# Optimization experiments

Hardware: AMD Instinct MI355X
Metric: run time of the kernel (lower is better)

## Reference

```python
import jax, jax.numpy as jnp
import numpy as np

DIM = 768
HEADS = 12
HEAD_DIM = DIM // HEADS
EPS_ATTN = 1e-6
LN_EPS = 1e-5


def _piece_weight():
    # BlockDistanceConv with num_patches_per_side=16, patch_group_size=16 -> 4x4 blocks
    bps = 4
    centers = np.array([[i + 0.5, j + 0.5] for i in range(bps) for j in range(bps)], dtype=np.float32)
    d = np.linalg.norm(centers[:, None, :] - centers[None, :, :], axis=-1)
    mat = np.cos(d / d.max() * np.pi / 4.0)  # 'cos' transform
    mat = mat / mat.sum(axis=0, keepdims=True)
    return jnp.asarray(mat, dtype=jnp.float32)  # [16, 16], out = W @ x over piece channels


def setup_inputs() -> dict:
    key = jax.random.key(0)
    ks = jax.random.split(key, 4)
    B, N, W, C = 128, 16, 16, DIM
    x = jax.random.normal(ks[0], (B, N, W, C), dtype=jnp.float32)
    ln_gamma = jnp.ones((C,), dtype=jnp.float32)
    ln_beta = jnp.zeros((C,), dtype=jnp.float32)
    w_qkv = jax.random.normal(ks[1], (C, 3 * C), dtype=jnp.float32) * (C ** -0.5)
    w_out = jax.random.normal(ks[2], (C, C), dtype=jnp.float32) * (C ** -0.5)
    b_out = jnp.zeros((C,), dtype=jnp.float32)
    w_piece = _piece_weight()
    return {"x": x, "ln_gamma": ln_gamma, "ln_beta": ln_beta, "w_qkv": w_qkv,
            "w_out": w_out, "b_out": b_out, "w_piece": w_piece}


def reference(x, ln_gamma, ln_beta, w_qkv, w_out, b_out, w_piece):
    B, N, W, C = x.shape
    H, D = HEADS, HEAD_DIM
    # LayerNorm over channel dim
    mu = jnp.mean(x, axis=-1, keepdims=True)
    var = jnp.mean((x - mu) ** 2, axis=-1, keepdims=True)
    xn = (x - mu) * jax.lax.rsqrt(var + LN_EPS) * ln_gamma + ln_beta
    # qkv projection (no bias)
    qkv = xn @ w_qkv  # [B,N,W,3C]
    q, k, v = jnp.split(qkv, 3, axis=-1)
    # relu kernel feature map
    q = jax.nn.relu(q) + EPS_ATTN
    k = jax.nn.relu(k) + EPS_ATTN
    # split heads: 'b n w (h d) -> b h n w d'
    def heads(t):
        return t.reshape(B, N, W, H, D).transpose(0, 3, 1, 2, 4)
    q, k, v = heads(q), heads(k), heads(v)
    # per-window kv = k^T v  (sum over window positions w)  -> [B,H,N,D,D]
    kv = jnp.einsum('bhnwd,bhnwe->bhnde', k, v)
    # BlockDistanceConv: 1x1 conv mixing over piece dim N with fixed weights
    kv = jnp.einsum('ij,bhjde->bhide', w_piece, kv)
    # out = q @ kv  -> [B,H,N,W,D]
    out = jnp.einsum('bhnwd,bhnde->bhnwe', q, kv)
    # merge heads: 'b h n w d -> b n w (h d)'
    out = out.transpose(0, 2, 3, 1, 4).reshape(B, N, W, H * D)
    # output projection (dropout is identity in eval)
    return out @ w_out + b_out
```

## Files before the change

### kernel.cpp

```cpp
#include <hip/hip_runtime.h>

#define DIM 768
#define HEADS 12
#define TOK 32768

typedef unsigned short ushort_t;
typedef __attribute__((ext_vector_type(8))) short short8v;
typedef __attribute__((ext_vector_type(4))) float f32x4;
typedef __attribute__((ext_vector_type(4))) unsigned short us4;

__device__ __forceinline__ ushort_t f2bf(float x) {
  union { float f; unsigned u; } c; c.f = x;
  unsigned r = (c.u + 0x7FFFu + ((c.u >> 16) & 1u)) >> 16;
  return (ushort_t)r;
}

__device__ __forceinline__ void gload_lds16(const void* g, void* l) {
  __builtin_amdgcn_global_load_lds((const __attribute__((address_space(1))) void*)g,
                                   (__attribute__((address_space(3))) void*)l, 16, 0, 0);
}

#define FENCE asm volatile("" ::: "memory")
#define SCHED0 __builtin_amdgcn_sched_barrier(0)
#define BARRIER do { FENCE; SCHED0; __builtin_amdgcn_s_barrier(); SCHED0; FENCE; } while (0)
#define LGK0 asm volatile("s_waitcnt lgkmcnt(0)" ::: "memory")
#define VM0  asm volatile("s_waitcnt vmcnt(0)" ::: "memory")
#define VM3  asm volatile("s_waitcnt vmcnt(3)" ::: "memory")

__global__ __launch_bounds__(256) void ln_kernel(const float* __restrict__ x,
                                                 const float* __restrict__ g,
                                                 const float* __restrict__ be,
                                                 ushort_t* __restrict__ xn) {
  int lane = threadIdx.x & 63;
  int row = blockIdx.x * 4 + (threadIdx.x >> 6);
  const float4* rx = (const float4*)(x + (size_t)row * DIM);
  float4 v[3];
  float s = 0.f, sq = 0.f;
  #pragma unroll
  for (int c = 0; c < 3; ++c) {
    v[c] = rx[lane + 64 * c];
    s  += v[c].x + v[c].y + v[c].z + v[c].w;
    sq += v[c].x * v[c].x + v[c].y * v[c].y + v[c].z * v[c].z + v[c].w * v[c].w;
  }
  #pragma unroll
  for (int off = 32; off; off >>= 1) {
    s  += __shfl_xor(s, off);
    sq += __shfl_xor(sq, off);
  }
  float mu  = s * (1.0f / DIM);
  float var = sq * (1.0f / DIM) - mu * mu;
  float rs  = rsqrtf(var + 1e-5f);
  us4* orow = (us4*)(xn + (size_t)row * DIM);
  const float4* gv = (const float4*)g;
  const float4* bv = (const float4*)be;
  #pragma unroll
  for (int c = 0; c < 3; ++c) {
    float4 gg = gv[lane + 64 * c];
    float4 bb = bv[lane + 64 * c];
    us4 pk;
    pk[0] = f2bf((v[c].x - mu) * rs * gg.x + bb.x);
    pk[1] = f2bf((v[c].y - mu) * rs * gg.y + bb.y);
    pk[2] = f2bf((v[c].z - mu) * rs * gg.z + bb.z);
    pk[3] = f2bf((v[c].w - mu) * rs * gg.w + bb.w);
    orow[lane + 64 * c] = pk;
  }
}

__global__ __launch_bounds__(256) void convT2(const float* __restrict__ s0,
                                              ushort_t* __restrict__ d0,
                                              const float* __restrict__ s1,
                                              ushort_t* __restrict__ d1) {
  int z = blockIdx.z;
  if (z && blockIdx.x >= DIM / 32) return;
  const float* src = z ? s1 : s0;
  ushort_t* dst = z ? d1 : d0;
  int Ccol = z ? DIM : 3 * DIM;
  const int R = DIM;
  __shared__ float tile[32][33];
  int c0 = blockIdx.x * 32, r0 = blockIdx.y * 32;
  int tx = threadIdx.x & 31, ty = threadIdx.x >> 5;
  #pragma unroll
  for (int i = 0; i < 32; i += 8)
    tile[ty + i][tx] = src[(size_t)(r0 + ty + i) * Ccol + c0 + tx];
  __syncthreads();
  #pragma unroll
  for (int i = 0; i < 32; i += 8)
    dst[(size_t)(c0 + ty + i) * R + r0 + tx] = f2bf(tile[tx][ty + i]);
}

__global__ __launch_bounds__(512, 4) void gemm_qkv(const ushort_t* __restrict__ A,
                                                   const ushort_t* __restrict__ Bt,
                                                   ushort_t* __restrict__ qbf,
                                                   ushort_t* __restrict__ kbf,
                                                   ushort_t* __restrict__ vTbf) {
  extern __shared__ __align__(16) char lds[];
  const int Kb = DIM * 2;
  const int N = 3 * DIM;
  const int nbn = N / 128;
  const int NT = DIM / 32;

  int bid = blockIdx.x;
  int qd = gridDim.x >> 3;
  int wid = (bid & 7) * qd + (bid >> 3);
  int bm = wid / nbn, bn = wid % nbn;
  int row0 = bm * 256, col0 = bn * 128;
  int t = threadIdx.x;
  int lane = t & 63, wave = t >> 6;
  int wr = wave >> 1, wc = wave & 1;

  const char* Ag = (const char*)A + (size_t)row0 * Kb;
  const char* Bg = (const char*)Bt + (size_t)col0 * Kb;

  int oA0 = t * 16, oA1 = 8192 + t * 16;
  int rA0 = oA0 >> 6, rA1 = oA1 >> 6;
  size_t gA0 = (size_t)rA0 * Kb + ((oA0 & 63) ^ (((rA0 >> 1) & 3) << 4));
  size_t gA1 = (size_t)rA1 * Kb + ((oA1 & 63) ^ (((rA1 >> 1) & 3) << 4));
  int oB = t * 16;
  int rB = oB >> 6;
  size_t gB = (size_t)rB * Kb + ((oB & 63) ^ (((rB >> 1) & 3) << 4));

  #define STG1(tile_, slot)                                                   \
    do {                                                                      \
      char* sb = lds + (slot) * 24576;                                        \
      size_t kk = (size_t)(tile_) * 64;                                       \
      gload_lds16(Ag + gA0 + kk, sb + oA0);                                   \
      gload_lds16(Ag + gA1 + kk, sb + oA1);                                   \
      gload_lds16(Bg + gB + kk, sb + 16384 + oB);                             \
    } while (0)

  int fr = lane & 15, fkb = (lane >> 4) << 4;
  int kb = fkb ^ (((fr >> 1) & 3) << 4);
  int aoff = (wr * 64 + fr) * 64 + kb;
  int boff = 16384 + (wc * 64 + fr) * 64 + kb;

  STG1(0, 0);

  f32x4 acc[4][4] = {};
  for (int kt = 0; kt < NT; ++kt) {
    int cur = kt & 1;
    if (kt + 1 < NT) { STG1(kt + 1, cur ^ 1); VM3; }
    else VM0;
    BARRIER;
    const char* sb = lds + cur * 24576;
    short8v a[4], b[4];
    #pragma unroll
    for (int mi = 0; mi < 4; ++mi) a[mi] = *(const short8v*)(sb + aoff + mi * 1024);
    #pragma unroll
    for (int ni = 0; ni < 4; ++ni) b[ni] = *(const short8v*)(sb + boff + ni * 1024);
    SCHED0;
    __builtin_amdgcn_s_setprio(1);
    #pragma unroll
    for (int mi = 0; mi < 4; ++mi)
      #pragma unroll
      for (int ni = 0; ni < 4; ++ni)
        acc[mi][ni] = __builtin_amdgcn_mfma_f32_16x16x32_bf16(a[mi], b[ni], acc[mi][ni], 0, 0, 0);
    __builtin_amdgcn_s_setprio(0);
    BARRIER;
  }
  #undef STG1

  int rbase = row0 + wr * 64 + ((lane >> 4) << 2);
  int cbase = col0 + wc * 64 + fr;
  #pragma unroll
  for (int m = 0; m < 4; ++m) {
    int r0r = rbase + m * 16;
    #pragma unroll
    for (int n = 0; n < 4; ++n) {
      int c = cbase + n * 16;
      if (c < DIM) {
        #pragma unroll
        for (int j = 0; j < 4; ++j)
          qbf[(size_t)(r0r + j) * DIM + c] = f2bf(fmaxf(acc[m][n][j], 0.0f) + 1e-6f);
      } else if (c < 2 * DIM) {
        #pragma unroll
        for (int j = 0; j < 4; ++j)
          kbf[(size_t)(r0r + j) * DIM + (c - DIM)] = f2bf(fmaxf(acc[m][n][j], 0.0f) + 1e-6f);
      } else {
        int ch = c - 2 * DIM;
        int hh = ch >> 6, e = ch & 63;
        int bb = r0r >> 8, rr = r0r & 255;
        us4 pk;
        #pragma unroll
        for (int j = 0; j < 4; ++j) pk[j] = f2bf(acc[m][n][j]);
        *(us4*)&vTbf[((((size_t)bb * HEADS + hh) * 64 + e) << 8) + rr] = pk;
      }
    }
  }
}

__global__ __launch_bounds__(512, 4) void gemm_out8(const ushort_t* __restrict__ A,
                                                    const ushort_t* __restrict__ Bt,
                                                    const float* __restrict__ bias,
                                                    float* __restrict__ C) {
  extern __shared__ __align__(16) char lds[];
  const int Kb = DIM * 2;
  const int N = DIM;
  const int nbn = N / 128;
  const int NT = DIM / 32;

  int bid = blockIdx.x;
  int qd = gridDim.x >> 3;
  int wid = (bid & 7) * qd + (bid >> 3);
  int bm = wid / nbn, bn = wid % nbn;
  int row0 = bm * 256, col0 = bn * 128;
  int t = threadIdx.x;
  int lane = t & 63, wave = t >> 6;
  int wr = wave >> 1, wc = wave & 1;

  const char* Ag = (const char*)A + (size_t)row0 * Kb;
  const char* Bg = (const char*)Bt + (size_t)col0 * Kb;

  int oA0 = t * 16, oA1 = 8192 + t * 16;
  int rA0 = oA0 >> 6, rA1 = oA1 >> 6;
  size_t gA0 = (size_t)rA0 * Kb + ((oA0 & 63) ^ (((rA0 >> 1) & 3) << 4));
  size_t gA1 = (size_t)rA1 * Kb + ((oA1 & 63) ^ (((rA1 >> 1) & 3) << 4));
  int oB = t * 16;
  int rB = oB >> 6;
  size_t gB = (size_t)rB * Kb + ((oB & 63) ^ (((rB >> 1) & 3) << 4));

  #define STG2(tile_, slot)                                                   \
    do {                                                                      \
      char* sb = lds + (slot) * 24576;                                        \
      size_t kk = (size_t)(tile_) * 64;                                       \
      gload_lds16(Ag + gA0 + kk, sb + oA0);                                   \
      gload_lds16(Ag + gA1 + kk, sb + oA1);                                   \
      gload_lds16(Bg + gB + kk, sb + 16384 + oB);                             \
    } while (0)

  int fr = lane & 15, fkb = (lane >> 4) << 4;
  int kb = fkb ^ (((fr >> 1) & 3) << 4);
  int aoff = (wr * 64 + fr) * 64 + kb;
  int boff = 16384 + (wc * 64 + fr) * 64 + kb;

  STG2(0, 0);

  f32x4 acc[4][4] = {};
  for (int kt = 0; kt < NT; ++kt) {
    int cur = kt & 1;
    if (kt + 1 < NT) { STG2(kt + 1, cur ^ 1); VM3; }
    else VM0;
    BARRIER;
    const char* sb = lds + cur * 24576;
    short8v a[4], b[4];
    #pragma unroll
    for (int mi = 0; mi < 4; ++mi) a[mi] = *(const short8v*)(sb + aoff + mi * 1024);
    #pragma unroll
    for (int ni = 0; ni < 4; ++ni) b[ni] = *(const short8v*)(sb + boff + ni * 1024);
    SCHED0;
    __builtin_amdgcn_s_setprio(1);
    #pragma unroll
    for (int mi = 0; mi < 4; ++mi)
      #pragma unroll
      for (int ni = 0; ni < 4; ++ni)
        acc[mi][ni] = __builtin_amdgcn_mfma_f32_16x16x32_bf16(a[mi], b[ni], acc[mi][ni], 0, 0, 0);
    __builtin_amdgcn_s_setprio(0);
    BARRIER;
  }
  #undef STG2

  int rbase = row0 + wr * 64 + ((lane >> 4) << 2);
  int cbase = col0 + wc * 64 + fr;
  #pragma unroll
  for (int m = 0; m < 4; ++m) {
    #pragma unroll
    for (int n = 0; n < 4; ++n) {
      int c = cbase + n * 16;
      float bz = bias[c];
      #pragma unroll
      for (int j = 0; j < 4; ++j)
        C[(size_t)(rbase + m * 16 + j) * N + c] = acc[m][n][j] + bz;
    }
  }
}

__global__ __launch_bounds__(512, 4) void attn_fused(const ushort_t* __restrict__ qbf,
                                                     const ushort_t* __restrict__ kbf,
                                                     const ushort_t* __restrict__ vTbf,
                                                     const float* __restrict__ wp,
                                                     ushort_t* __restrict__ attnO) {
  extern __shared__ __align__(16) char lds[];
  const int QOFF = 32768, SOFF = 40960;
  int bh = blockIdx.x;
  int b = bh / HEADS, h = bh % HEADS;
  int t = threadIdx.x;
  int lane = t & 63, wave = t >> 6;
  int fr = lane & 15, fkb = (lane >> 4) << 4;
  int lg4 = (lane >> 4) << 2;

  const char* qg = (const char*)(qbf + ((size_t)b * 256) * DIM + h * 64);
  const char* kg = (const char*)(kbf + ((size_t)b * 256) * DIM + h * 64);
  const char* vg = (const char*)(vTbf + ((size_t)bh << 14));

  #pragma unroll
  for (int is = 0; is < 4; ++is) {
    int o = is * 8192 + t * 16;
    int r = o >> 7;
    int byt = (o & 127) ^ ((r & 7) << 4);
    gload_lds16(kg + (size_t)r * (DIM * 2) + byt, lds + o);
  }
  {
    int o = t * 16;
    int r = o >> 7;
    int byt = (o & 127) ^ ((r & 7) << 4);
    gload_lds16(qg + (size_t)r * (DIM * 2) + byt, lds + QOFF + o);
  }
  #pragma unroll
  for (int is = 0; is < 4; ++is) {
    int o = is * 8192 + t * 16;
    int e = o >> 9;
    int byt = (o & 511) ^ ((e & 7) << 4);
    gload_lds16(vg + e * 512 + byt, lds + SOFF + o);
  }
  VM0;
  __builtin_amdgcn_s_barrier();

  int wrs = wave & 3, wcs = wave >> 2;
  int wrp = wave >> 2, wcp = wave & 3;

  short8v vt[8];
  {
    int e = wcp * 16 + fr;
    int es = (e & 7) << 4;
    #pragma unroll
    for (int ks = 0; ks < 8; ++ks)
      vt[ks] = *(const short8v*)(lds + SOFF + e * 512 + ((ks * 64 + fkb) ^ es));
  }
  LGK0;
  BARRIER;

  for (int q4 = 0; q4 < 4; ++q4) {
    f32x4 accA[4][2] = {};
    {
      short8v qf[2][2];
      #pragma unroll
      for (int ni = 0; ni < 2; ++ni) {
        int r = wcs * 32 + ni * 16 + fr;
        int rs = (r & 7) << 4;
        qf[ni][0] = *(const short8v*)(lds + QOFF + r * 128 + (fkb ^ rs));
        qf[ni][1] = *(const short8v*)(lds + QOFF + r * 128 + ((64 + fkb) ^ rs));
      }
      #pragma unroll
      for (int mi = 0; mi < 4; ++mi) {
        int r = wrs * 64 + mi * 16 + fr;
        int rs = (r & 7) << 4;
        short8v kf0 = *(const short8v*)(lds + r * 128 + (fkb ^ rs));
        short8v kf1 = *(const short8v*)(lds + r * 128 + ((64 + fkb) ^ rs));
        #pragma unroll
        for (int ni = 0; ni < 2; ++ni) {
          accA[mi][ni] = __builtin_amdgcn_mfma_f32_16x16x32_bf16(kf0, qf[ni][0], accA[mi][ni], 0, 0, 0);
          accA[mi][ni] = __builtin_amdgcn_mfma_f32_16x16x32_bf16(kf1, qf[ni][1], accA[mi][ni], 0, 0, 0);
        }
      }
    }
    BARRIER;
    #pragma unroll
    for (int mi = 0; mi < 4; ++mi)
      #pragma unroll
      for (int ni = 0; ni < 2; ++ni) {
        float wpf = wp[(q4 * 4 + wcs * 2 + ni) * 16 + wrs * 4 + mi];
        us4 pk;
        #pragma unroll
        for (int j = 0; j < 4; ++j) pk[j] = f2bf(accA[mi][ni][j] * wpf);
        int qrow = wcs * 32 + ni * 16 + fr;
        int sbyte = (wrs * 64 + mi * 16 + lg4) * 2;
        *(us4*)(lds + SOFF + qrow * 512 + (sbyte ^ ((qrow & 7) << 4))) = pk;
      }
    if (q4 < 3) {
      int o = t * 16;
      int r = o >> 7;
      int byt = (o & 127) ^ ((r & 7) << 4);
      gload_lds16(qg + (size_t)((q4 + 1) * 64 + r) * (DIM * 2) + byt, lds + QOFF + o);
    }
    LGK0;
    BARRIER;
    f32x4 accB[2] = {{0.f,0.f,0.f,0.f},{0.f,0.f,0.f,0.f}};
    #pragma unroll
    for (int ks = 0; ks < 8; ++ks) {
      int kbq = ks * 64 + fkb;
      #pragma unroll
      for (int mt = 0; mt < 2; ++mt) {
        int r = wrp * 32 + mt * 16 + fr;
        short8v av = *(const short8v*)(lds + SOFF + r * 512 + (kbq ^ ((r & 7) << 4)));
        accB[mt] = __builtin_amdgcn_mfma_f32_16x16x32_bf16(av, vt[ks], accB[mt], 0, 0, 0);
      }
    }
    #pragma unroll
    for (int mt = 0; mt < 2; ++mt) {
      int row = b * 256 + q4 * 64 + wrp * 32 + mt * 16 + lg4;
      int col = h * 64 + wcp * 16 + fr;
      #pragma unroll
      for (int j = 0; j < 4; ++j)
        attnO[(size_t)(row + j) * DIM + col] = f2bf(accB[mt][j]);
    }
    if (q4 < 3) asm volatile("s_waitcnt vmcnt(8)" ::: "memory");
    BARRIER;
  }
}

extern "C" void kernel_launch(void* const* d_in, const int* in_sizes, int n_in,
                              void* d_out, int out_size, void* d_ws, size_t ws_size,
                              hipStream_t stream) {
  const float* x    = (const float*)d_in[0];
  const float* g    = (const float*)d_in[1];
  const float* be   = (const float*)d_in[2];
  const float* wqkv = (const float*)d_in[3];
  const float* wout = (const float*)d_in[4];
  const float* bout = (const float*)d_in[5];
  const float* wp   = (const float*)d_in[6];
  float* out = (float*)d_out;

  char* w = (char*)d_ws;
  const size_t SZ = (size_t)TOK * DIM * 2;
  ushort_t* qbf   = (ushort_t*)(w);
  ushort_t* kbf   = (ushort_t*)(w + SZ);
  ushort_t* vTbf  = (ushort_t*)(w + 2 * SZ);
  ushort_t* xn    = (ushort_t*)(w + 3 * SZ);
  ushort_t* wqkvT = (ushort_t*)(w + 4 * SZ);
  ushort_t* woutT = (ushort_t*)(w + 4 * SZ + 3538944);
  ushort_t* attnO = xn;

  (void)hipFuncSetAttribute(reinterpret_cast<const void*>(&gemm_qkv),
                            hipFuncAttributeMaxDynamicSharedMemorySize, 49152);
  (void)hipFuncSetAttribute(reinterpret_cast<const void*>(&gemm_out8),
                            hipFuncAttributeMaxDynamicSharedMemorySize, 49152);
  (void)hipFuncSetAttribute(reinterpret_cast<const void*>(&attn_fused),
                            hipFuncAttributeMaxDynamicSharedMemorySize, 73728);

  dim3 gct(3 * DIM / 32, DIM / 32, 2);
  convT2<<<gct, 256, 0, stream>>>(wqkv, wqkvT, wout, woutT);

  ln_kernel<<<TOK / 4, 256, 0, stream>>>(x, g, be, xn);

  gemm_qkv<<<(TOK / 256) * (3 * DIM / 128), 512, 49152, stream>>>(
      xn, wqkvT, qbf, kbf, vTbf);

  attn_fused<<<128 * HEADS, 512, 73728, stream>>>(qbf, kbf, vTbf, wp, attnO);

  gemm_out8<<<(TOK / 256) * (DIM / 128), 512, 49152, stream>>>(
      attnO, woutT, bout, out);
}
```

Measured before the change: 269.6 us.

## Load QKV GEMM B operand directly to registers and hoist K fragments in attention

In the QKV GEMM, the weight (B) tile is no longer staged through LDS. Each wave loads its B fragments straight into double-buffered registers with inline global_load_dwordx4, which shrinks LDS per block from 48KB to 32KB and removes the B-side LDS reads. In the attention kernel, the K fragments are loaded from LDS once before the q4 loop instead of on every iteration. The cost is more register pressure, and B rows are now read redundantly from global memory by waves that share a column (via cache), with no LDS reuse across waves.

```diff
diff --git a/kernel.cpp b/kernel.cpp
--- a/kernel.cpp
+++ b/kernel.cpp
@@ -26,6 +26,7 @@
 #define LGK0 asm volatile("s_waitcnt lgkmcnt(0)" ::: "memory")
 #define VM0  asm volatile("s_waitcnt vmcnt(0)" ::: "memory")
 #define VM3  asm volatile("s_waitcnt vmcnt(3)" ::: "memory")
+#define VM6  asm volatile("s_waitcnt vmcnt(6)" ::: "memory")
 
 __global__ __launch_bounds__(256) void ln_kernel(const float* __restrict__ x,
                                                  const float* __restrict__ g,
@@ -109,55 +110,65 @@
   int wr = wave >> 1, wc = wave & 1;
 
   const char* Ag = (const char*)A + (size_t)row0 * Kb;
-  const char* Bg = (const char*)Bt + (size_t)col0 * Kb;
 
   int oA0 = t * 16, oA1 = 8192 + t * 16;
   int rA0 = oA0 >> 6, rA1 = oA1 >> 6;
   size_t gA0 = (size_t)rA0 * Kb + ((oA0 & 63) ^ (((rA0 >> 1) & 3) << 4));
   size_t gA1 = (size_t)rA1 * Kb + ((oA1 & 63) ^ (((rA1 >> 1) & 3) << 4));
-  int oB = t * 16;
-  int rB = oB >> 6;
-  size_t gB = (size_t)rB * Kb + ((oB & 63) ^ (((rB >> 1) & 3) << 4));
 
   #define STG1(tile_, slot)                                                   \
     do {                                                                      \
-      char* sb = lds + (slot) * 24576;                                        \
+      char* sb = lds + (slot) * 16384;                                        \
       size_t kk = (size_t)(tile_) * 64;                                       \
       gload_lds16(Ag + gA0 + kk, sb + oA0);                                   \
       gload_lds16(Ag + gA1 + kk, sb + oA1);                                   \
-      gload_lds16(Bg + gB + kk, sb + 16384 + oB);                             \
     } while (0)
 
   int fr = lane & 15, fkb = (lane >> 4) << 4;
   int kb = fkb ^ (((fr >> 1) & 3) << 4);
   int aoff = (wr * 64 + fr) * 64 + kb;
-  int boff = 16384 + (wc * 64 + fr) * 64 + kb;
-
+
+  const char* vB = (const char*)Bt + (size_t)(col0 + wc * 64 + fr) * Kb + fkb;
+
+  short8v bb[2][4];
+  #define BLOAD(buf, kt_)                                                     \
+    _Pragma("unroll") for (int ni = 0; ni < 4; ++ni)                          \
+      asm volatile("global_load_dwordx4 %0, %1, off"                          \
+                   : "=&v"(bb[buf][ni])                                       \
+                   : "v"(vB + (size_t)(ni) * 16 * Kb + (size_t)(kt_) * 64)    \
+                   : "memory");
+
+  BLOAD(0, 0);
   STG1(0, 0);
 
   f32x4 acc[4][4] = {};
+  #pragma unroll
   for (int kt = 0; kt < NT; ++kt) {
-    int cur = kt & 1;
-    if (kt + 1 < NT) { STG1(kt + 1, cur ^ 1); VM3; }
-    else VM0;
-    BARRIER;
-    const char* sb = lds + cur * 24576;
-    short8v a[4], b[4];
+    const int cur = kt & 1;
+    if (kt + 1 < NT) {
+      BLOAD(cur ^ 1, kt + 1);
+      STG1(kt + 1, cur ^ 1);
+      VM6;
+    } else {
+      VM0;
+    }
+    BARRIER;
+    const char* sb = lds + cur * 16384;
+    short8v a[4];
     #pragma unroll
     for (int mi = 0; mi < 4; ++mi) a[mi] = *(const short8v*)(sb + aoff + mi * 1024);
-    #pragma unroll
-    for (int ni = 0; ni < 4; ++ni) b[ni] = *(const short8v*)(sb + boff + ni * 1024);
     SCHED0;
     __builtin_amdgcn_s_setprio(1);
     #pragma unroll
     for (int mi = 0; mi < 4; ++mi)
       #pragma unroll
       for (int ni = 0; ni < 4; ++ni)
-        acc[mi][ni] = __builtin_amdgcn_mfma_f32_16x16x32_bf16(a[mi], b[ni], acc[mi][ni], 0, 0, 0);
+        acc[mi][ni] = __builtin_amdgcn_mfma_f32_16x16x32_bf16(a[mi], bb[cur][ni], acc[mi][ni], 0, 0, 0);
     __builtin_amdgcn_s_setprio(0);
     BARRIER;
   }
   #undef STG1
+  #undef BLOAD
 
   int rbase = row0 + wr * 64 + ((lane >> 4) << 2);
   int cbase = col0 + wc * 64 + fr;
@@ -178,11 +189,11 @@
       } else {
         int ch = c - 2 * DIM;
         int hh = ch >> 6, e = ch & 63;
-        int bb = r0r >> 8, rr = r0r & 255;
+        int bb2 = r0r >> 8, rr = r0r & 255;
         us4 pk;
         #pragma unroll
         for (int j = 0; j < 4; ++j) pk[j] = f2bf(acc[m][n][j]);
-        *(us4*)&vTbf[((((size_t)bb * HEADS + hh) * 64 + e) << 8) + rr] = pk;
+        *(us4*)&vTbf[((((size_t)bb2 * HEADS + hh) * 64 + e) << 8) + rr] = pk;
       }
     }
   }
@@ -325,6 +336,14 @@
     for (int ks = 0; ks < 8; ++ks)
       vt[ks] = *(const short8v*)(lds + SOFF + e * 512 + ((ks * 64 + fkb) ^ es));
   }
+  short8v kf[4][2];
+  #pragma unroll
+  for (int mi = 0; mi < 4; ++mi) {
+    int r = wrs * 64 + mi * 16 + fr;
+    int rs = (r & 7) << 4;
+    kf[mi][0] = *(const short8v*)(lds + r * 128 + (fkb ^ rs));
+    kf[mi][1] = *(const short8v*)(lds + r * 128 + ((64 + fkb) ^ rs));
+  }
   LGK0;
   BARRIER;
 
@@ -340,17 +359,12 @@
         qf[ni][1] = *(const short8v*)(lds + QOFF + r * 128 + ((64 + fkb) ^ rs));
       }
       #pragma unroll
-      for (int mi = 0; mi < 4; ++mi) {
-        int r = wrs * 64 + mi * 16 + fr;
-        int rs = (r & 7) << 4;
-        short8v kf0 = *(const short8v*)(lds + r * 128 + (fkb ^ rs));
-        short8v kf1 = *(const short8v*)(lds + r * 128 + ((64 + fkb) ^ rs));
+      for (int mi = 0; mi < 4; ++mi)
         #pragma unroll
         for (int ni = 0; ni < 2; ++ni) {
-          accA[mi][ni] = __builtin_amdgcn_mfma_f32_16x16x32_bf16(kf0, qf[ni][0], accA[mi][ni], 0, 0, 0);
-          accA[mi][ni] = __builtin_amdgcn_mfma_f32_16x16x32_bf16(kf1, qf[ni][1], accA[mi][ni], 0, 0, 0);
+          accA[mi][ni] = __builtin_amdgcn_mfma_f32_16x16x32_bf16(kf[mi][0], qf[ni][0], accA[mi][ni], 0, 0, 0);
+          accA[mi][ni] = __builtin_amdgcn_mfma_f32_16x16x32_bf16(kf[mi][1], qf[ni][1], accA[mi][ni], 0, 0, 0);
         }
-      }
     }
     BARRIER;
     #pragma unroll
@@ -420,7 +434,7 @@
   ushort_t* attnO = xn;
 
   (void)hipFuncSetAttribute(reinterpret_cast<const void*>(&gemm_qkv),
-                            hipFuncAttributeMaxDynamicSharedMemorySize, 49152);
+                            hipFuncAttributeMaxDynamicSharedMemorySize, 32768);
   (void)hipFuncSetAttribute(reinterpret_cast<const void*>(&gemm_out8),
                             hipFuncAttributeMaxDynamicSharedMemorySize, 49152);
   (void)hipFuncSetAttribute(reinterpret_cast<const void*>(&attn_fused),
@@ -431,7 +445,7 @@
 
   ln_kernel<<<TOK / 4, 256, 0, stream>>>(x, g, be, xn);
 
-  gemm_qkv<<<(TOK / 256) * (3 * DIM / 128), 512, 49152, stream>>>(
+  gemm_qkv<<<(TOK / 256) * (3 * DIM / 128), 512, 32768, stream>>>(
       xn, wqkvT, qbf, kbf, vTbf);
 
   attn_fused<<<128 * HEADS, 512, 73728, stream>>>(qbf, kbf, vTbf, wp, attnO);
```

Measured after the change: 391.0 us. 45.0% more time.

## Shrink out-projection GEMM tile and overlap V load with first attention score GEMM

Applied to the files above, without the earlier changes.

The output GEMM now uses 128x128 tiles with 256 threads and 32KB of LDS instead of 256x128 with 512 threads, which doubles the grid and should raise occupancy. In the fused attention kernel, the first K·Q score GEMM starts while the V transpose loads are still in flight. The score GEMM for each following query chunk is moved to the end of the previous iteration, so it overlaps with outstanding loads. The costs are more blocks re-reading the B tile and subtler vmcnt and barrier ordering, with a risk of race bugs.

```diff
diff --git a/kernel.cpp b/kernel.cpp
--- a/kernel.cpp
+++ b/kernel.cpp
@@ -26,6 +26,7 @@
 #define LGK0 asm volatile("s_waitcnt lgkmcnt(0)" ::: "memory")
 #define VM0  asm volatile("s_waitcnt vmcnt(0)" ::: "memory")
 #define VM3  asm volatile("s_waitcnt vmcnt(3)" ::: "memory")
+#define VM4  asm volatile("s_waitcnt vmcnt(4)" ::: "memory")
 
 __global__ __launch_bounds__(256) void ln_kernel(const float* __restrict__ x,
                                                  const float* __restrict__ g,
@@ -188,7 +189,7 @@
   }
 }
 
-__global__ __launch_bounds__(512, 4) void gemm_out8(const ushort_t* __restrict__ A,
+__global__ __launch_bounds__(256, 4) void gemm_out8(const ushort_t* __restrict__ A,
                                                     const ushort_t* __restrict__ Bt,
                                                     const float* __restrict__ bias,
                                                     float* __restrict__ C) {
@@ -202,7 +203,7 @@
   int qd = gridDim.x >> 3;
   int wid = (bid & 7) * qd + (bid >> 3);
   int bm = wid / nbn, bn = wid % nbn;
-  int row0 = bm * 256, col0 = bn * 128;
+  int row0 = bm * 128, col0 = bn * 128;
   int t = threadIdx.x;
   int lane = t & 63, wave = t >> 6;
   int wr = wave >> 1, wc = wave & 1;
@@ -210,37 +211,35 @@
   const char* Ag = (const char*)A + (size_t)row0 * Kb;
   const char* Bg = (const char*)Bt + (size_t)col0 * Kb;
 
-  int oA0 = t * 16, oA1 = 8192 + t * 16;
-  int rA0 = oA0 >> 6, rA1 = oA1 >> 6;
-  size_t gA0 = (size_t)rA0 * Kb + ((oA0 & 63) ^ (((rA0 >> 1) & 3) << 4));
-  size_t gA1 = (size_t)rA1 * Kb + ((oA1 & 63) ^ (((rA1 >> 1) & 3) << 4));
-  int oB = t * 16;
-  int rB = oB >> 6;
-  size_t gB = (size_t)rB * Kb + ((oB & 63) ^ (((rB >> 1) & 3) << 4));
+  int o0 = t * 16, o1 = 4096 + t * 16;
+  int r0s = o0 >> 6, r1s = o1 >> 6;
+  size_t g0 = (size_t)r0s * Kb + ((o0 & 63) ^ (((r0s >> 1) & 3) << 4));
+  size_t g1 = (size_t)r1s * Kb + ((o1 & 63) ^ (((r1s >> 1) & 3) << 4));
 
   #define STG2(tile_, slot)                                                   \
     do {                                                                      \
-      char* sb = lds + (slot) * 24576;                                        \
+      char* sb = lds + (slot) * 16384;                                        \
       size_t kk = (size_t)(tile_) * 64;                                       \
-      gload_lds16(Ag + gA0 + kk, sb + oA0);                                   \
-      gload_lds16(Ag + gA1 + kk, sb + oA1);                                   \
-      gload_lds16(Bg + gB + kk, sb + 16384 + oB);                             \
+      gload_lds16(Ag + g0 + kk, sb + o0);                                     \
+      gload_lds16(Ag + g1 + kk, sb + o1);                                     \
+      gload_lds16(Bg + g0 + kk, sb + 8192 + o0);                              \
+      gload_lds16(Bg + g1 + kk, sb + 8192 + o1);                              \
     } while (0)
 
   int fr = lane & 15, fkb = (lane >> 4) << 4;
   int kb = fkb ^ (((fr >> 1) & 3) << 4);
   int aoff = (wr * 64 + fr) * 64 + kb;
-  int boff = 16384 + (wc * 64 + fr) * 64 + kb;
+  int boff = 8192 + (wc * 64 + fr) * 64 + kb;
 
   STG2(0, 0);
 
   f32x4 acc[4][4] = {};
   for (int kt = 0; kt < NT; ++kt) {
     int cur = kt & 1;
-    if (kt + 1 < NT) { STG2(kt + 1, cur ^ 1); VM3; }
+    if (kt + 1 < NT) { STG2(kt + 1, cur ^ 1); VM4; }
     else VM0;
     BARRIER;
-    const char* sb = lds + cur * 24576;
+    const char* sb = lds + cur * 16384;
     short8v a[4], b[4];
     #pragma unroll
     for (int mi = 0; mi < 4; ++mi) a[mi] = *(const short8v*)(sb + aoff + mi * 1024);
@@ -311,11 +310,39 @@
     int byt = (o & 511) ^ ((e & 7) << 4);
     gload_lds16(vg + e * 512 + byt, lds + SOFF + o);
   }
-  VM0;
+  VM4;
   __builtin_amdgcn_s_barrier();
 
   int wrs = wave & 3, wcs = wave >> 2;
   int wrp = wave >> 2, wcp = wave & 3;
+
+  #define SGEMM_BODY(accA_)                                                     \
+    do {                                                                        \
+      short8v qf[2][2];                                                         \
+      _Pragma("unroll") for (int ni = 0; ni < 2; ++ni) {                        \
+        int r = wcs * 32 + ni * 16 + fr;                                        \
+        int rs = (r & 7) << 4;                                                  \
+        qf[ni][0] = *(const short8v*)(lds + QOFF + r * 128 + (fkb ^ rs));       \
+        qf[ni][1] = *(const short8v*)(lds + QOFF + r * 128 + ((64 + fkb) ^ rs));\
+      }                                                                         \
+      _Pragma("unroll") for (int mi = 0; mi < 4; ++mi) {                        \
+        int r = wrs * 64 + mi * 16 + fr;                                        \
+        int rs = (r & 7) << 4;                                                  \
+        short8v kf0 = *(const short8v*)(lds + r * 128 + (fkb ^ rs));            \
+        short8v kf1 = *(const short8v*)(lds + r * 128 + ((64 + fkb) ^ rs));     \
+        _Pragma("unroll") for (int ni = 0; ni < 2; ++ni) {                      \
+          accA_[mi][ni] = __builtin_amdgcn_mfma_f32_16x16x32_bf16(              \
+              kf0, qf[ni][0], accA_[mi][ni], 0, 0, 0);                          \
+          accA_[mi][ni] = __builtin_amdgcn_mfma_f32_16x16x32_bf16(              \
+              kf1, qf[ni][1], accA_[mi][ni], 0, 0, 0);                          \
+        }                                                                       \
+      }                                                                         \
+    } while (0)
+
+  f32x4 accA[4][2] = {};
+  SGEMM_BODY(accA);
+  VM0;
+  BARRIER;
 
   short8v vt[8];
   {
@@ -329,30 +356,6 @@
   BARRIER;
 
   for (int q4 = 0; q4 < 4; ++q4) {
-    f32x4 accA[4][2] = {};
-    {
-      short8v qf[2][2];
-      #pragma unroll
-      for (int ni = 0; ni < 2; ++ni) {
-        int r = wcs * 32 + ni * 16 + fr;
-        int rs = (r & 7) << 4;
-        qf[ni][0] = *(const short8v*)(lds + QOFF + r * 128 + (fkb ^ rs));
-        qf[ni][1] = *(const short8v*)(lds + QOFF + r * 128 + ((64 + fkb) ^ rs));
-      }
-      #pragma unroll
-      for (int mi = 0; mi < 4; ++mi) {
-        int r = wrs * 64 + mi * 16 + fr;
-        int rs = (r & 7) << 4;
-        short8v kf0 = *(const short8v*)(lds + r * 128 + (fkb ^ rs));
-        short8v kf1 = *(const short8v*)(lds + r * 128 + ((64 + fkb) ^ rs));
-        #pragma unroll
-        for (int ni = 0; ni < 2; ++ni) {
-          accA[mi][ni] = __builtin_amdgcn_mfma_f32_16x16x32_bf16(kf0, qf[ni][0], accA[mi][ni], 0, 0, 0);
-          accA[mi][ni] = __builtin_amdgcn_mfma_f32_16x16x32_bf16(kf1, qf[ni][1], accA[mi][ni], 0, 0, 0);
-        }
-      }
-    }
-    BARRIER;
     #pragma unroll
     for (int mi = 0; mi < 4; ++mi)
       #pragma unroll
@@ -392,9 +395,18 @@
       for (int j = 0; j < 4; ++j)
         attnO[(size_t)(row + j) * DIM + col] = f2bf(accB[mt][j]);
     }
-    if (q4 < 3) asm volatile("s_waitcnt vmcnt(8)" ::: "memory");
-    BARRIER;
-  }
+    if (q4 < 3) {
+      asm volatile("s_waitcnt vmcnt(8)" ::: "memory");
+      BARRIER;
+      #pragma unroll
+      for (int mi = 0; mi < 4; ++mi)
+        #pragma unroll
+        for (int ni = 0; ni < 2; ++ni) accA[mi][ni] = f32x4{0.f, 0.f, 0.f, 0.f};
+      SGEMM_BODY(accA);
+      BARRIER;
+    }
+  }
+  #undef SGEMM_BODY
 }
 
 extern "C" void kernel_launch(void* const* d_in, const int* in_sizes, int n_in,
@@ -422,7 +434,7 @@
   (void)hipFuncSetAttribute(reinterpret_cast<const void*>(&gemm_qkv),
                             hipFuncAttributeMaxDynamicSharedMemorySize, 49152);
   (void)hipFuncSetAttribute(reinterpret_cast<const void*>(&gemm_out8),
-                            hipFuncAttributeMaxDynamicSharedMemorySize, 49152);
+                            hipFuncAttributeMaxDynamicSharedMemorySize, 32768);
   (void)hipFuncSetAttribute(reinterpret_cast<const void*>(&attn_fused),
                             hipFuncAttributeMaxDynamicSharedMemorySize, 73728);
 
@@ -436,6 +448,6 @@
 
   attn_fused<<<128 * HEADS, 512, 73728, stream>>>(qbf, kbf, vTbf, wp, attnO);
 
-  gemm_out8<<<(TOK / 256) * (DIM / 128), 512, 49152, stream>>>(
+  gemm_out8<<<(TOK / 128) * (DIM / 128), 256, 32768, stream>>>(
       attnO, woutT, bout, out);
 }
```

After: 271.2 us (median of 2 runs). About the same (+0.6%).
